# Kernel tuning notes

Hardware: AMD Instinct MI355X
Metric: run time of the kernel (lower is better)

Reference implementation:

```python
import jax, jax.numpy as jnp
import numpy as np

DIM = 128
HEADS = DIM // 8      # mala uses dim//8 heads
HEAD_DIM = 8
HID = int(DIM * 2.66) # 340
B, H, W = 8, 128, 128


def _ln(x, w, b):
    # WithBias LayerNorm over channel dim of NCHW (per-pixel)
    mu = jnp.mean(x, axis=1, keepdims=True)
    var = jnp.mean((x - mu) ** 2, axis=1, keepdims=True)
    return (x - mu) / jnp.sqrt(var + 1e-5) * w[None, :, None, None] + b[None, :, None, None]


def _conv1x1(x, w):
    return jnp.einsum('bchw,oc->bohw', x, w)


def _dwconv(x, w, pad):
    return jax.lax.conv_general_dilated(
        x, w, (1, 1), ((pad, pad), (pad, pad)),
        dimension_numbers=('NCHW', 'OIHW', 'NCHW'),
        feature_group_count=x.shape[1])


def _rope(h, w, head_dim, dtype):
    angle = 1.0 / 10000 ** jnp.linspace(0.0, 1.0, head_dim // 4, dtype=dtype)
    angle = jnp.repeat(angle, 2)                                  # [d/2]
    ih = jnp.arange(h, dtype=dtype)[:, None] * angle[None, :]     # [h, d/2]
    iw = jnp.arange(w, dtype=dtype)[:, None] * angle[None, :]     # [w, d/2]
    d2 = head_dim // 2
    sin = jnp.concatenate([jnp.broadcast_to(jnp.sin(ih)[:, None, :], (h, w, d2)),
                           jnp.broadcast_to(jnp.sin(iw)[None, :, :], (h, w, d2))], -1)
    cos = jnp.concatenate([jnp.broadcast_to(jnp.cos(ih)[:, None, :], (h, w, d2)),
                           jnp.broadcast_to(jnp.cos(iw)[None, :, :], (h, w, d2))], -1)
    return sin.reshape(h * w, head_dim), cos.reshape(h * w, head_dim)


def _rot2(x):
    x1 = x[..., 0::2]
    x2 = x[..., 1::2]
    return jnp.stack([-x2, x1], axis=-1).reshape(x.shape)


def _theta_shift(x, sin, cos):
    return x * cos + _rot2(x) * sin


def setup_inputs() -> dict:
    key = jax.random.key(0)
    ks = jax.random.split(key, 8)
    f = jnp.float32
    return {
        'x': jax.random.normal(ks[0], (B, DIM, H, W), f),
        'ln1_w': jnp.ones((DIM,), f), 'ln1_b': jnp.zeros((DIM,), f),
        'qkvo_w': jax.random.normal(ks[1], (4 * DIM, DIM), f) * (DIM ** -0.5),
        'qkvo_b': jnp.zeros((4 * DIM,), f),
        'lepe_w': jax.random.normal(ks[2], (DIM, 1, 5, 5), f) * 0.2,
        'lepe_b': jnp.zeros((DIM,), f),
        'proj_w': jax.random.normal(ks[3], (DIM, DIM), f) * (DIM ** -0.5),
        'proj_b': jnp.zeros((DIM,), f),
        'ln2_w': jnp.ones((DIM,), f), 'ln2_b': jnp.zeros((DIM,), f),
        'ffn_in_w': jax.random.normal(ks[4], (2 * HID, DIM), f) * (DIM ** -0.5),
        'ffn_dw_w': jax.random.normal(ks[5], (2 * HID, 1, 3, 3), f) * (1.0 / 3.0),
        'ffn_out_w': jax.random.normal(ks[6], (DIM, HID), f) * (HID ** -0.5),
    }


def reference(x, ln1_w, ln1_b, qkvo_w, qkvo_b, lepe_w, lepe_b, proj_w, proj_b,
              ln2_w, ln2_b, ffn_in_w, ffn_dw_w, ffn_out_w):
    Bx, C, Hh, Ww = x.shape
    L = Hh * Ww
    n, d = HEADS, HEAD_DIM
    scale = d ** -0.5

    # --- MALA branch ---
    xn = _ln(x, ln1_w, ln1_b)
    sin, cos = _rope(Hh, Ww, d, x.dtype)
    qkvo = _conv1x1(xn, qkvo_w) + qkvo_b[None, :, None, None]       # [B,4C,H,W]
    qkv, o = qkvo[:, :3 * C], qkvo[:, 3 * C:]
    lepe = _dwconv(qkv[:, 2 * C:], lepe_w, 2) + lepe_b[None, :, None, None]
    t = qkv.reshape(Bx, 3, n, d, L).transpose(1, 0, 2, 4, 3)         # [3,B,n,L,d]
    q = jax.nn.elu(t[0]) + 1.0
    k = jax.nn.elu(t[1]) + 1.0
    v = t[2]
    # z = q @ mean_l(k)^T * scale  (pre-RoPE features)
    z = jnp.einsum('bnld,bnd->bnl', q, jnp.mean(k, axis=2))[..., None] * scale  # [B,n,L,1]
    q = _theta_shift(q, sin, cos)
    k = _theta_shift(k, sin, cos)
    kv = jnp.einsum('bnld,bnle->bnde', k, v) * (scale / L)           # [B,n,d,d]
    res = jnp.einsum('bnld,bnde->bnle', q, kv) * (1.0 + 1.0 / (z + 1e-6)) \
          - z * jnp.mean(v, axis=2, keepdims=True)                   # [B,n,L,d]
    res = res.transpose(0, 1, 3, 2).reshape(Bx, C, Hh, Ww) + lepe
    attn = _conv1x1(res * o, proj_w) + proj_b[None, :, None, None]
    x = x + attn

    # --- gated dwconv FFN ---
    xn2 = _ln(x, ln2_w, ln2_b)
    p = _dwconv(_conv1x1(xn2, ffn_in_w), ffn_dw_w, 1)                # [B,2*HID,H,W]
    x1, x2 = p[:, :HID], p[:, HID:]
    x = x + _conv1x1(jax.nn.gelu(x1, approximate=False) * x2, ffn_out_w)
    return x
```

## Files before the change

### kernel.cpp

```cpp
#include <hip/hip_runtime.h>

#define LSP 16384
#define NBATCH 8
#define NPOS (NBATCH*LSP)
#define NHID 340
#define ATT_SCALE 0.35355339059327373f

#define OFF_A        0ULL
#define OFF_B        33554432ULL
#define OFF_GT2      79691776ULL
#define OFF_C        100663296ULL
#define OFF_PART     134217728ULL
#define OFF_STATS    134381568ULL
#define OFF_SIN      134422528ULL
#define OFF_COS      134946816ULL
#define OFF_WQ       135471104ULL
#define OFF_WQO      135602176ULL
#define OFF_QOB      135667712ULL
#define OFF_WP       135668736ULL
#define OFF_WFI      135701504ULL
#define OFF_WFO      135881728ULL
#define WS_NEEDED    135971840ULL

typedef __attribute__((ext_vector_type(8))) short short8;
typedef __attribute__((ext_vector_type(4))) float floatx4;

__device__ __forceinline__ float bf2f(unsigned short u){
  union { unsigned int i; float f; } c; c.i = ((unsigned int)u) << 16; return c.f;
}
__device__ __forceinline__ unsigned short f2bf(float f){
  union { float f; unsigned int i; } c; c.f = f;
  unsigned int r = c.i + 0x7fffu + ((c.i >> 16) & 1u);
  return (unsigned short)(r >> 16);
}

__device__ __forceinline__ void load_row12(const unsigned short* p, float* r){
  const unsigned int* q = (const unsigned int*)p;
  #pragma unroll
  for (int i=0;i<6;i++){
    unsigned int u = q[i];
    r[2*i]   = bf2f((unsigned short)(u & 0xffffu));
    r[2*i+1] = bf2f((unsigned short)(u >> 16));
  }
}

__device__ __forceinline__ void load_row10(const unsigned short* base, float* r){
  short8 B = *(const short8*)(base + 8);
  r[0] = bf2f(base[7]);
  #pragma unroll
  for (int i=0;i<8;i++) r[1+i] = bf2f((unsigned short)B[i]);
  r[9] = bf2f(base[16]);
}

__global__ void rope_kernel(float* __restrict__ sin_t, float* __restrict__ cos_t){
  int l = blockIdx.x*256 + threadIdx.x;
  if (l >= LSP) return;
  int h = l >> 7, w = l & 127;
  float s0 = sinf((float)h),        c0 = cosf((float)h);
  float s1 = sinf((float)h*1e-4f),  c1 = cosf((float)h*1e-4f);
  float s2 = sinf((float)w),        c2 = cosf((float)w);
  float s3 = sinf((float)w*1e-4f),  c3 = cosf((float)w*1e-4f);
  float* sp = sin_t + l*8; float* cp = cos_t + l*8;
  sp[0]=s0; sp[1]=s0; sp[2]=s1; sp[3]=s1; sp[4]=s2; sp[5]=s2; sp[6]=s3; sp[7]=s3;
  cp[0]=c0; cp[1]=c0; cp[2]=c1; cp[3]=c1; cp[4]=c2; cp[5]=c2; cp[6]=c3; cp[7]=c3;
}

__global__ void wconv_kernel(const float* __restrict__ src, unsigned short* __restrict__ dst,
                             int O, int K, int OP, int KP){
  int i = blockIdx.x*256 + threadIdx.x;
  if (i >= OP*KP) return;
  int o = i / KP, k = i - o*KP;
  float v = (o < O && k < K) ? src[o*K + k] : 0.f;
  dst[i] = f2bf(v);
}

__global__ void reorder_qo_kernel(const float* __restrict__ qkvo_w, const float* __restrict__ qkvo_b,
                                  unsigned short* __restrict__ wqo, float* __restrict__ qo_bias){
  int i = blockIdx.x*256 + threadIdx.x;
  if (i < 256){
    qo_bias[i] = qkvo_b[(i < 128) ? i : i + 256];
  }
  if (i >= 256*128) return;
  int o = i >> 7, k = i & 127;
  int srow = (o < 128) ? o : o + 256;
  wqo[i] = f2bf(qkvo_w[srow*128 + k]);
}

__launch_bounds__(256)
__global__ void ln_kernel(const float* __restrict__ x, const float* __restrict__ gam,
                          const float* __restrict__ bet, unsigned short* __restrict__ out_t){
  __shared__ float ps[2][128], pq[2][128];
  __shared__ unsigned short tile[128*132];
  int t = threadIdx.x;
  int pidx = t & 127;
  int half = t >> 7;
  int p0 = blockIdx.x*128;
  int p = p0 + pidx;
  int b = p >> 14, l = p & 16383;
  const float* xb = x + (((size_t)b) << 21) + (((size_t)(half*64)) << 14) + l;
  float vals[64];
  float s = 0.f, sq = 0.f;
  #pragma unroll
  for (int c = 0; c < 64; c++){
    float v = xb[(size_t)c << 14];
    vals[c] = v;
    s += v; sq += v*v;
  }
  ps[half][pidx] = s; pq[half][pidx] = sq;
  __syncthreads();
  float S = ps[0][pidx] + ps[1][pidx];
  float Q = pq[0][pidx] + pq[1][pidx];
  float mu = S * 0.0078125f;
  float var = Q * 0.0078125f - mu*mu;
  float rstd = rsqrtf(var + 1e-5f);
  #pragma unroll
  for (int c0 = 0; c0 < 64; c0 += 8){
    short8 vv;
    #pragma unroll
    for (int i = 0; i < 8; i++){
      int c = c0 + i;
      int cg = half*64 + c;
      vv[i] = (short)f2bf((vals[c] - mu) * rstd * gam[cg] + bet[cg]);
    }
    *(short8*)&tile[pidx*132 + half*64 + c0] = vv;
  }
  __syncthreads();
  unsigned short* og = out_t + ((size_t)p0 << 7);
  #pragma unroll
  for (int it = 0; it < 8; it++){
    int idx = it*256 + t;
    int row = idx >> 4;
    int col = (idx & 15) * 8;
    *(short8*)&og[(row << 7) + col] = *(const short8*)&tile[row*132 + col];
  }
}

template<int OPAD, int KPAD, bool HASBIAS, bool RESID, bool OUTBF16>
__launch_bounds__(256)
__global__ void gemm_kernel(const unsigned short* __restrict__ in_t,
                            const unsigned short* __restrict__ wb,
                            const float* __restrict__ bias,
                            const float* __restrict__ resid,
                            void* __restrict__ outp){
  constexpr int KS = KPAD / 32;
  constexpr int SBYTES = OUTBF16 ? (64*136*2) : (64*132*4);
  __shared__ __align__(16) unsigned char smem[SBYTES];
  const int l0 = blockIdx.x * 128;
  const int b = l0 >> 14;
  const int lloc0 = l0 & 16383;
  const int t = threadIdx.x;
  const int lane = t & 63;
  const int wv = t >> 6;
  const int lane15 = lane & 15;
  const int quad = lane >> 4;
  const int oc = blockIdx.y;

  short8 fb[2][KS];
  {
    const unsigned short* base = in_t + ((size_t)(l0 + wv*32 + lane15)) * KPAD + quad*8;
    #pragma unroll
    for (int nt = 0; nt < 2; nt++){
      #pragma unroll
      for (int ks = 0; ks < KS; ks++)
        fb[nt][ks] = *(const short8*)(base + (size_t)nt*16*KPAD + ks*32);
    }
  }
  floatx4 acc[4][2];
  #pragma unroll
  for (int mt=0; mt<4; mt++)
    #pragma unroll
    for (int nt=0; nt<2; nt++)
      acc[mt][nt] = (floatx4){0.f,0.f,0.f,0.f};
  #pragma unroll
  for (int ks = 0; ks < KS; ks++){
    short8 fa[4];
    const unsigned short* wrow = wb + ((size_t)(oc*64 + lane15)) * KPAD + ks*32 + quad*8;
    #pragma unroll
    for (int mt=0; mt<4; mt++)
      fa[mt] = *(const short8*)(wrow + (size_t)mt*16*KPAD);
    #pragma unroll
    for (int mt=0; mt<4; mt++)
      #pragma unroll
      for (int nt=0; nt<2; nt++)
        acc[mt][nt] = __builtin_amdgcn_mfma_f32_16x16x32_bf16(fa[mt], fb[nt][ks], acc[mt][nt], 0, 0, 0);
  }

  if (OUTBF16){
    unsigned short* cs = (unsigned short*)smem;
    #pragma unroll
    for (int mt=0; mt<4; mt++)
      #pragma unroll
      for (int nt=0; nt<2; nt++)
        #pragma unroll
        for (int r=0; r<4; r++){
          const int o = mt*16 + quad*4 + r;
          float v = acc[mt][nt][r];
          if (HASBIAS) v += bias[oc*64 + o];
          cs[o*136 + wv*32 + nt*16 + lane15] = f2bf(v);
        }
    __syncthreads();
    unsigned short* og = (unsigned short*)outp;
    #pragma unroll
    for (int j=0; j<4; j++){
      int idx = j*256 + t;
      int row = idx >> 4;
      int col = (idx & 15) * 8;
      short8 v = *(const short8*)&cs[row*136 + col];
      *(short8*)&og[(((size_t)(b*OPAD + oc*64 + row)) << 14) + lloc0 + col] = v;
    }
  } else {
    float* cf = (float*)smem;
    #pragma unroll
    for (int mt=0; mt<4; mt++)
      #pragma unroll
      for (int nt=0; nt<2; nt++)
        #pragma unroll
        for (int r=0; r<4; r++){
          const int o = mt*16 + quad*4 + r;
          float v = acc[mt][nt][r];
          if (HASBIAS) v += bias[oc*64 + o];
          cf[o*132 + wv*32 + nt*16 + lane15] = v;
        }
    __syncthreads();
    float* og = (float*)outp;
    #pragma unroll
    for (int j=0; j<8; j++){
      int idx = j*256 + t;
      int row = idx >> 5;
      int col = (idx & 31) * 4;
      floatx4 v = *(const floatx4*)&cf[row*132 + col];
      if (RESID){
        floatx4 rv = *(const floatx4*)(resid + (((size_t)(b*128 + oc*64 + row)) << 14) + lloc0 + col);
        v += rv;
      }
      *(floatx4*)&og[(((size_t)(b*OPAD + oc*64 + row)) << 14) + lloc0 + col] = v;
    }
  }
}

__launch_bounds__(256)
__global__ void lepe_kernel(const unsigned short* __restrict__ kv,
                            const float* __restrict__ lw, const float* __restrict__ lb,
                            unsigned short* __restrict__ lepe){
  __shared__ unsigned short lds[132*136];
  int bc = blockIdx.x;
  int b = bc >> 7, c = bc & 127;
  int t = threadIdx.x;
  #pragma unroll
  for (int i = t; i < 132*136/8; i += 256)
    *(short8*)(lds + i*8) = (short8){0,0,0,0,0,0,0,0};
  __syncthreads();
  int band = t >> 4, wi = t & 15, w0 = wi*8;
  const unsigned short* vp = kv + (((size_t)(b*256 + 128 + c)) << 14);
  {
    #pragma unroll
    for (int it = 0; it < 8; it++){
      int hh = band + it*16;
      short8 v = *(const short8*)(vp + (hh<<7) + w0);
      unsigned int* dst = (unsigned int*)&lds[(hh+2)*136 + w0 + 2];
      union { short8 s; unsigned int u[4]; } cv; cv.s = v;
      #pragma unroll
      for (int q=0;q<4;q++) dst[q] = cv.u[q];
    }
  }
  float wt[25];
  #pragma unroll
  for (int i=0;i<25;i++) wt[i] = lw[c*25 + i];
  float bias = lb[c];
  __syncthreads();
  int h0 = band*8;
  float win[5][12];
  #pragma unroll
  for (int m=0;m<4;m++) load_row12(&lds[(h0+m)*136 + w0], win[m]);
  unsigned short* outp = lepe + ((size_t)bc << 14);
  #pragma unroll
  for (int s=0;s<8;s++){
    load_row12(&lds[(h0+4+s)*136 + w0], win[(4+s)%5]);
    short8 ov;
    #pragma unroll
    for (int j=0;j<8;j++){
      float acc = bias;
      #pragma unroll
      for (int dy=0;dy<5;dy++){
        const float* r = win[(s+dy)%5];
        #pragma unroll
        for (int dx=0;dx<5;dx++) acc += wt[dy*5+dx]*r[j+dx];
      }
      ov[j] = (short)f2bf(acc);
    }
    *(short8*)(outp + (h0+s)*128 + w0) = ov;
  }
}

__launch_bounds__(256)
__global__ void attn_partial(const unsigned short* __restrict__ kv,
                             const float* __restrict__ sin_t, const float* __restrict__ cos_t,
                             float* __restrict__ partials){
  int pair = blockIdx.x >> 2;
  int chunk = blockIdx.x & 3;
  int b = pair >> 4, hd = pair & 15;
  const unsigned short* kb = kv + (((size_t)(b*256 + hd*8)) << 14);
  const unsigned short* vb = kb + ((size_t)128 << 14);
  float red[80];
  #pragma unroll
  for (int i=0;i<80;i++) red[i]=0.f;
  int l0 = chunk*4096;
  for (int li=0; li<16; li++){
    int l = l0 + li*256 + threadIdx.x;
    float k[8], v[8], ks[8];
    #pragma unroll
    for (int e=0;e<8;e++){
      float t = bf2f(kb[((size_t)e<<14)+l]);
      k[e] = t>0.f ? t+1.f : __expf(t);
      v[e] = bf2f(vb[((size_t)e<<14)+l]);
      red[e]   += k[e];
      red[8+e] += v[e];
    }
    const float* sp = sin_t + l*8;
    const float* cp = cos_t + l*8;
    #pragma unroll
    for (int j=0;j<4;j++){
      float x1=k[2*j], x2=k[2*j+1];
      ks[2*j]   = x1*cp[2*j]   - x2*sp[2*j];
      ks[2*j+1] = x2*cp[2*j+1] + x1*sp[2*j+1];
    }
    #pragma unroll
    for (int d=0; d<8; d++)
      #pragma unroll
      for (int e=0;e<8;e++)
        red[16 + d*8 + e] += ks[d]*v[e];
  }
  #pragma unroll
  for (int off=32; off>0; off>>=1){
    #pragma unroll
    for (int i=0;i<80;i++)
      red[i] += __shfl_down(red[i], off);
  }
  __shared__ float lds[4][80];
  int lane = threadIdx.x & 63, wv = threadIdx.x >> 6;
  if (lane==0){
    #pragma unroll
    for (int i=0;i<80;i++) lds[wv][i] = red[i];
  }
  __syncthreads();
  if (threadIdx.x < 80){
    float s = lds[0][threadIdx.x]+lds[1][threadIdx.x]+lds[2][threadIdx.x]+lds[3][threadIdx.x];
    partials[(size_t)blockIdx.x*80 + threadIdx.x] = s;
  }
}

__global__ void attn_combine(const float* __restrict__ partials, float* __restrict__ stats){
  int i = blockIdx.x*256 + threadIdx.x;
  if (i >= 128*80) return;
  int pair = i / 80, idx = i - pair*80;
  float s = partials[(size_t)(pair*4+0)*80+idx] + partials[(size_t)(pair*4+1)*80+idx]
          + partials[(size_t)(pair*4+2)*80+idx] + partials[(size_t)(pair*4+3)*80+idx];
  s *= (idx < 16) ? (1.f/LSP) : (ATT_SCALE/LSP);
  stats[i] = s;
}

__launch_bounds__(256)
__global__ void attn_apply_kernel(const unsigned short* __restrict__ qo,
                                  const unsigned short* __restrict__ lepe,
                                  const float* __restrict__ stats,
                                  const float* __restrict__ sin_t,
                                  const float* __restrict__ cos_t,
                                  unsigned short* __restrict__ resg_t){
  __shared__ float st[16*80];
  __shared__ unsigned short tile[256*132];
  int p0 = blockIdx.x * 256;
  int b = p0 >> 14;
  for (int i = threadIdx.x; i < 16*80; i += 256) st[i] = stats[b*16*80 + i];
  __syncthreads();
  int t = threadIdx.x;
  int p = p0 + t;
  int l = p & 16383;
  float sv[8], cv[8];
  {
    const float* sp = sin_t + l*8;
    const float* cp = cos_t + l*8;
    #pragma unroll
    for (int i=0;i<8;i++){ sv[i]=sp[i]; cv[i]=cp[i]; }
  }
  #pragma unroll 1
  for (int hd=0; hd<16; hd++){
    const float* S = st + hd*80;
    const unsigned short* qb = qo + (((size_t)(b*256 + hd*8)) << 14) + l;
    const unsigned short* ob = qb + ((size_t)128 << 14);
    const unsigned short* lb = lepe + (((size_t)(b*128 + hd*8)) << 14) + l;
    float q[8];
    #pragma unroll
    for (int e=0;e<8;e++){
      float tq = bf2f(qb[(size_t)e<<14]);
      q[e] = tq > 0.f ? tq + 1.f : __expf(tq);
    }
    float z = 0.f;
    #pragma unroll
    for (int e=0;e<8;e++) z += q[e]*S[e];
    z *= ATT_SCALE;
    float qs[8];
    #pragma unroll
    for (int jj=0;jj<4;jj++){
      float x1=q[2*jj], x2=q[2*jj+1];
      qs[2*jj]   = x1*cv[2*jj]   - x2*sv[2*jj];
      qs[2*jj+1] = x2*cv[2*jj+1] + x1*sv[2*jj+1];
    }
    float fac = 1.f + 1.f/(z + 1e-6f);
    short8 vv;
    #pragma unroll
    for (int e=0;e<8;e++){
      float r = 0.f;
      #pragma unroll
      for (int d=0; d<8; d++) r += qs[d]*S[16 + d*8 + e];
      r = r*fac - z*S[8+e];
      float val = (r + bf2f(lb[(size_t)e<<14])) * bf2f(ob[(size_t)e<<14]);
      vv[e] = (short)f2bf(val);
    }
    *(short8*)&tile[t*132 + hd*8] = vv;
  }
  __syncthreads();
  unsigned short* og = resg_t + ((size_t)p0 << 7);
  #pragma unroll
  for (int it = 0; it < 16; it++){
    int idx = it*256 + t;
    int row = idx >> 4;
    int col = (idx & 15) * 8;
    *(short8*)&og[(row << 7) + col] = *(const short8*)&tile[row*132 + col];
  }
}

#define FPL (66*144)
__launch_bounds__(256)
__global__ void ffn_dwg_kernel(const unsigned short* __restrict__ p,
                               const float* __restrict__ dw,
                               unsigned short* __restrict__ g){
  __shared__ unsigned short lds[2*FPL];
  int bid = blockIdx.x;
  int jc = bid % NHID;
  int rest = bid / NHID;
  int bb = rest & 1;
  int half = rest >> 1;
  int t = threadIdx.x;
  #pragma unroll
  for (int i = t; i < 2*FPL/8; i += 256)
    *(short8*)(lds + i*8) = (short8){0,0,0,0,0,0,0,0};
  __syncthreads();
  int band = t >> 4, wi = t & 15, w0 = wi*8;
  #pragma unroll
  for (int pl=0; pl<2; pl++){
    const unsigned short* src = p + (((size_t)(bb*704 + jc + pl*NHID)) << 14);
    #pragma unroll
    for (int it=0; it<5; it++){
      int r_idx = it*16 + band;
      if (r_idx < 66){
        int h = half*64 - 1 + r_idx;
        if ((unsigned)h < 128u){
          short8 v = *(const short8*)(src + (h<<7) + w0);
          *(short8*)(&lds[pl*FPL + r_idx*144 + w0 + 8]) = v;
        }
      }
    }
  }
  float w1[9], w2[9];
  #pragma unroll
  for (int i=0;i<9;i++){ w1[i] = dw[jc*9 + i]; w2[i] = dw[(jc+NHID)*9 + i]; }
  __syncthreads();
  int rb = band*4;
  float r1[3][10], r2[3][10];
  #pragma unroll
  for (int m=0;m<2;m++){
    load_row10(&lds[(rb+m)*144 + w0], r1[m]);
    load_row10(&lds[FPL + (rb+m)*144 + w0], r2[m]);
  }
  unsigned short* outp = g + (((size_t)(bb*NHID + jc)) << 14);
  #pragma unroll
  for (int s=0;s<4;s++){
    load_row10(&lds[(rb+2+s)*144 + w0], r1[(2+s)%3]);
    load_row10(&lds[FPL + (rb+2+s)*144 + w0], r2[(2+s)%3]);
    int h = half*64 + rb + s;
    short8 ov;
    #pragma unroll
    for (int j=0;j<8;j++){
      float c1 = 0.f, c2 = 0.f;
      #pragma unroll
      for (int dy=0;dy<3;dy++){
        const float* a = r1[(s+dy)%3];
        const float* bpt = r2[(s+dy)%3];
        #pragma unroll
        for (int dx=0;dx<3;dx++){
          c1 += w1[dy*3+dx]*a[j+dx];
          c2 += w2[dy*3+dx]*bpt[j+dx];
        }
      }
      float ge = 0.5f*c1*(1.f + erff(c1*0.70710678118654752f));
      ov[j] = (short)f2bf(ge*c2);
    }
    *(short8*)(outp + h*128 + w0) = ov;
  }
}

__global__ void transpose_g_kernel(const unsigned short* __restrict__ g,
                                   unsigned short* __restrict__ g_t){
  __shared__ unsigned short tile[64][68];
  int bid = blockIdx.x;
  int jt = bid % 6;
  int lt = (bid / 6) & 255;
  int b  = bid / (6*256);
  int j0 = jt*64, l0 = lt*64;
  int t = threadIdx.x;
  {
    int jj = t >> 3;
    int lo = (t & 7) * 8;
    #pragma unroll
    for (int rr=0; rr<2; rr++){
      int j = j0 + jj + rr*32;
      unsigned short vals[8];
      if (j < NHID){
        const unsigned short* src = g + (((size_t)(b*NHID + j)) << 14) + l0 + lo;
        short8 vv = *(const short8*)src;
        #pragma unroll
        for (int i=0;i<8;i++) vals[i] = (unsigned short)vv[i];
      } else {
        #pragma unroll
        for (int i=0;i<8;i++) vals[i] = 0;
      }
      #pragma unroll
      for (int i=0;i<8;i++) tile[lo + i][jj + rr*32] = vals[i];
    }
  }
  __syncthreads();
  {
    int r = t >> 2;
    int c0 = (t & 3)*16;
    int jg = j0 + c0;
    if (jg < 352){
      unsigned short* dst = g_t + ((size_t)(b*LSP + l0 + r))*352 + jg;
      short8 v0, v1;
      #pragma unroll
      for (int i=0;i<8;i++){ v0[i] = (short)tile[r][c0 + i]; v1[i] = (short)tile[r][c0 + 8 + i]; }
      *(short8*)dst = v0;
      *(short8*)(dst+8) = v1;
    }
  }
}

extern "C" void kernel_launch(void* const* d_in, const int* in_sizes, int n_in,
                              void* d_out, int out_size, void* d_ws, size_t ws_size,
                              hipStream_t stream){
  (void)in_sizes; (void)n_in; (void)out_size;
  if (ws_size < WS_NEEDED) return;
  const float* x        = (const float*)d_in[0];
  const float* ln1_w    = (const float*)d_in[1];
  const float* ln1_b    = (const float*)d_in[2];
  const float* qkvo_w   = (const float*)d_in[3];
  const float* qkvo_b   = (const float*)d_in[4];
  const float* lepe_w   = (const float*)d_in[5];
  const float* lepe_b   = (const float*)d_in[6];
  const float* proj_w   = (const float*)d_in[7];
  const float* proj_b   = (const float*)d_in[8];
  const float* ln2_w    = (const float*)d_in[9];
  const float* ln2_b    = (const float*)d_in[10];
  const float* ffn_in_w = (const float*)d_in[11];
  const float* ffn_dw_w = (const float*)d_in[12];
  const float* ffn_out_w= (const float*)d_in[13];

  char* ws = (char*)d_ws;
  unsigned short* bufA   = (unsigned short*)(ws + OFF_A);
  unsigned short* bufB   = (unsigned short*)(ws + OFF_B);
  unsigned short* g_t2   = (unsigned short*)(ws + OFF_GT2);
  unsigned short* lepe   = (unsigned short*)(ws + OFF_C);
  unsigned short* gbuf   = (unsigned short*)(ws + OFF_C);
  float* partials        = (float*)(ws + OFF_PART);
  float* stats           = (float*)(ws + OFF_STATS);
  float* sin_t           = (float*)(ws + OFF_SIN);
  float* cos_t           = (float*)(ws + OFF_COS);
  unsigned short* wq     = (unsigned short*)(ws + OFF_WQ);
  unsigned short* wqo    = (unsigned short*)(ws + OFF_WQO);
  float* qo_bias         = (float*)(ws + OFF_QOB);
  unsigned short* wp     = (unsigned short*)(ws + OFF_WP);
  unsigned short* wfi    = (unsigned short*)(ws + OFF_WFI);
  unsigned short* wfo    = (unsigned short*)(ws + OFF_WFO);
  const unsigned short* wkv = wq + 128*128;

  float* out_f = (float*)d_out;
  dim3 blk(256);
  hipLaunchKernelGGL(rope_kernel, dim3(64), blk, 0, stream, sin_t, cos_t);
  hipLaunchKernelGGL(wconv_kernel, dim3((512*128)/256), blk, 0, stream, qkvo_w, wq, 512,128,512,128);
  hipLaunchKernelGGL(reorder_qo_kernel, dim3((256*128)/256), blk, 0, stream, qkvo_w, qkvo_b, wqo, qo_bias);
  hipLaunchKernelGGL(wconv_kernel, dim3((128*128)/256), blk, 0, stream, proj_w, wp, 128,128,128,128);
  hipLaunchKernelGGL(wconv_kernel, dim3((704*128)/256), blk, 0, stream, ffn_in_w, wfi, 680,128,704,128);
  hipLaunchKernelGGL(wconv_kernel, dim3((128*352)/256), blk, 0, stream, ffn_out_w, wfo, 128,340,128,352);

  hipLaunchKernelGGL(ln_kernel, dim3(1024), blk, 0, stream, x, ln1_w, ln1_b, bufA);
  hipLaunchKernelGGL((gemm_kernel<256,128,true,false,true>), dim3(1024,4), blk, 0, stream,
                     bufA, wkv, qkvo_b + 128, (const float*)nullptr, (void*)bufB);
  hipLaunchKernelGGL(lepe_kernel, dim3(1024), blk, 0, stream, bufB, lepe_w, lepe_b, lepe);
  hipLaunchKernelGGL(attn_partial, dim3(512), blk, 0, stream, bufB, sin_t, cos_t, partials);
  hipLaunchKernelGGL(attn_combine, dim3(40), blk, 0, stream, partials, stats);
  hipLaunchKernelGGL((gemm_kernel<256,128,true,false,true>), dim3(1024,4), blk, 0, stream,
                     bufA, wqo, qo_bias, (const float*)nullptr, (void*)bufB);
  hipLaunchKernelGGL(attn_apply_kernel, dim3(512), blk, 0, stream, bufB, lepe, stats, sin_t, cos_t, bufA);
  hipLaunchKernelGGL((gemm_kernel<128,128,true,true,false>), dim3(1024,2), blk, 0, stream,
                     bufA, wp, proj_b, x, (void*)out_f);

  hipLaunchKernelGGL(ln_kernel, dim3(1024), blk, 0, stream, out_f, ln2_w, ln2_b, bufA);
  for (int bp = 0; bp < 4; bp++){
    const unsigned short* xin = bufA + (size_t)bp*32768*128;
    float* outp = out_f + (size_t)bp*2*128*16384;
    hipLaunchKernelGGL((gemm_kernel<704,128,false,false,true>), dim3(256,11), blk, 0, stream,
                       xin, wfi, (const float*)nullptr, (const float*)nullptr, (void*)bufB);
    hipLaunchKernelGGL(ffn_dwg_kernel, dim3(1360), blk, 0, stream, bufB, ffn_dw_w, gbuf);
    hipLaunchKernelGGL(transpose_g_kernel, dim3(3072), blk, 0, stream, gbuf, g_t2);
    hipLaunchKernelGGL((gemm_kernel<128,352,false,true,false>), dim3(256,2), blk, 0, stream,
                       g_t2, wfo, (const float*)nullptr, outp, (void*)outp);
  }
}
```

Measured before the change: 728.6 us.

## Fuse FFN gate transpose into output GEMM and split attention kernels wider

```diff
diff --git a/kernel.cpp b/kernel.cpp
--- a/kernel.cpp
+++ b/kernel.cpp
@@ -239,6 +239,91 @@
 }
 
 __launch_bounds__(256)
+__global__ void ffn_out_gemm(const unsigned short* __restrict__ g,
+                             const unsigned short* __restrict__ wb,
+                             float* __restrict__ outp){
+  __shared__ __align__(16) unsigned char smem[64*132*4];
+  const int t = threadIdx.x;
+  const int l0 = blockIdx.x * 128;
+  const int b = l0 >> 14;
+  const int lloc0 = l0 & 16383;
+  const int lane = t & 63;
+  const int wv = t >> 6;
+  const int lane15 = lane & 15;
+  const int quad = lane >> 4;
+  const int oc = blockIdx.y;
+  const int jj = t >> 3;
+  const int c8 = t & 7;
+
+  auto stage = [&](int s, int bufi){
+    unsigned short* buf = (unsigned short*)(smem + bufi*10240);
+    int j = s*32 + jj;
+    const unsigned short* src = g + (((size_t)(b*NHID + j)) << 14) + lloc0;
+    #pragma unroll
+    for (int cc=0; cc<2; cc++){
+      int c = c8 + cc*8;
+      short8 v = (short8){0,0,0,0,0,0,0,0};
+      if (j < NHID) v = *(const short8*)(src + c*8);
+      #pragma unroll
+      for (int e=0; e<8; e++)
+        buf[(c*8+e)*40 + jj] = (unsigned short)v[e];
+    }
+  };
+
+  floatx4 acc[4][2];
+  #pragma unroll
+  for (int mt=0; mt<4; mt++)
+    #pragma unroll
+    for (int nt=0; nt<2; nt++)
+      acc[mt][nt] = (floatx4){0.f,0.f,0.f,0.f};
+
+  stage(0, 0);
+  #pragma unroll 1
+  for (int s=0; s<11; s++){
+    __syncthreads();
+    if (s < 10) stage(s+1, (s+1)&1);
+    const unsigned short* cur = (const unsigned short*)(smem + (s&1)*10240);
+    short8 fbv[2];
+    #pragma unroll
+    for (int nt=0; nt<2; nt++)
+      fbv[nt] = *(const short8*)&cur[(wv*32 + nt*16 + lane15)*40 + quad*8];
+    const unsigned short* wrow = wb + ((size_t)(oc*64 + lane15))*352 + s*32 + quad*8;
+    short8 fa[4];
+    #pragma unroll
+    for (int mt=0; mt<4; mt++)
+      fa[mt] = *(const short8*)(wrow + (size_t)mt*16*352);
+    #pragma unroll
+    for (int mt=0; mt<4; mt++)
+      #pragma unroll
+      for (int nt=0; nt<2; nt++)
+        acc[mt][nt] = __builtin_amdgcn_mfma_f32_16x16x32_bf16(fa[mt], fbv[nt], acc[mt][nt], 0, 0, 0);
+  }
+  __syncthreads();
+  float* cf = (float*)smem;
+  #pragma unroll
+  for (int mt=0; mt<4; mt++)
+    #pragma unroll
+    for (int nt=0; nt<2; nt++)
+      #pragma unroll
+      for (int r=0; r<4; r++){
+        const int o = mt*16 + quad*4 + r;
+        cf[o*132 + wv*32 + nt*16 + lane15] = acc[mt][nt][r];
+      }
+  __syncthreads();
+  #pragma unroll
+  for (int j=0; j<8; j++){
+    int idx = j*256 + t;
+    int row = idx >> 5;
+    int col = (idx & 31) * 4;
+    floatx4 v = *(const floatx4*)&cf[row*132 + col];
+    size_t oi = (((size_t)(b*128 + oc*64 + row)) << 14) + lloc0 + col;
+    floatx4 rv = *(const floatx4*)&outp[oi];
+    v += rv;
+    *(floatx4*)&outp[oi] = v;
+  }
+}
+
+__launch_bounds__(256)
 __global__ void lepe_kernel(const unsigned short* __restrict__ kv,
                             const float* __restrict__ lw, const float* __restrict__ lb,
                             unsigned short* __restrict__ lepe){
@@ -296,16 +381,16 @@
 __global__ void attn_partial(const unsigned short* __restrict__ kv,
                              const float* __restrict__ sin_t, const float* __restrict__ cos_t,
                              float* __restrict__ partials){
-  int pair = blockIdx.x >> 2;
-  int chunk = blockIdx.x & 3;
+  int pair = blockIdx.x >> 3;
+  int chunk = blockIdx.x & 7;
   int b = pair >> 4, hd = pair & 15;
   const unsigned short* kb = kv + (((size_t)(b*256 + hd*8)) << 14);
   const unsigned short* vb = kb + ((size_t)128 << 14);
   float red[80];
   #pragma unroll
   for (int i=0;i<80;i++) red[i]=0.f;
-  int l0 = chunk*4096;
-  for (int li=0; li<16; li++){
+  int l0 = chunk*2048;
+  for (int li=0; li<8; li++){
     int l = l0 + li*256 + threadIdx.x;
     float k[8], v[8], ks[8];
     #pragma unroll
@@ -353,8 +438,10 @@
   int i = blockIdx.x*256 + threadIdx.x;
   if (i >= 128*80) return;
   int pair = i / 80, idx = i - pair*80;
-  float s = partials[(size_t)(pair*4+0)*80+idx] + partials[(size_t)(pair*4+1)*80+idx]
-          + partials[(size_t)(pair*4+2)*80+idx] + partials[(size_t)(pair*4+3)*80+idx];
+  float s = 0.f;
+  #pragma unroll
+  for (int cc=0; cc<8; cc++)
+    s += partials[(size_t)(pair*8+cc)*80+idx];
   s *= (idx < 16) ? (1.f/LSP) : (ATT_SCALE/LSP);
   stats[i] = s;
 }
@@ -366,11 +453,12 @@
                                   const float* __restrict__ sin_t,
                                   const float* __restrict__ cos_t,
                                   unsigned short* __restrict__ resg_t){
-  __shared__ float st[16*80];
-  __shared__ unsigned short tile[256*132];
+  __shared__ float st[8*80];
+  __shared__ unsigned short tile[256*66];
   int p0 = blockIdx.x * 256;
   int b = p0 >> 14;
-  for (int i = threadIdx.x; i < 16*80; i += 256) st[i] = stats[b*16*80 + i];
+  int hg = blockIdx.y;
+  for (int i = threadIdx.x; i < 8*80; i += 256) st[i] = stats[b*16*80 + hg*8*80 + i];
   __syncthreads();
   int t = threadIdx.x;
   int p = p0 + t;
@@ -383,8 +471,9 @@
     for (int i=0;i<8;i++){ sv[i]=sp[i]; cv[i]=cp[i]; }
   }
   #pragma unroll 1
-  for (int hd=0; hd<16; hd++){
-    const float* S = st + hd*80;
+  for (int hd8=0; hd8<8; hd8++){
+    int hd = hg*8 + hd8;
+    const float* S = st + hd8*80;
     const unsigned short* qb = qo + (((size_t)(b*256 + hd*8)) << 14) + l;
     const unsigned short* ob = qb + ((size_t)128 << 14);
     const unsigned short* lb = lepe + (((size_t)(b*128 + hd*8)) << 14) + l;
@@ -416,16 +505,16 @@
       float val = (r + bf2f(lb[(size_t)e<<14])) * bf2f(ob[(size_t)e<<14]);
       vv[e] = (short)f2bf(val);
     }
-    *(short8*)&tile[t*132 + hd*8] = vv;
-  }
-  __syncthreads();
-  unsigned short* og = resg_t + ((size_t)p0 << 7);
-  #pragma unroll
-  for (int it = 0; it < 16; it++){
+    *(short8*)&tile[t*66 + hd8*8] = vv;
+  }
+  __syncthreads();
+  unsigned short* og = resg_t + ((size_t)p0 << 7) + hg*64;
+  #pragma unroll
+  for (int it = 0; it < 8; it++){
     int idx = it*256 + t;
-    int row = idx >> 4;
-    int col = (idx & 15) * 8;
-    *(short8*)&og[(row << 7) + col] = *(const short8*)&tile[row*132 + col];
+    int row = idx >> 3;
+    int col = (idx & 7) * 8;
+    *(short8*)&og[(row << 7) + col] = *(const short8*)&tile[row*66 + col];
   }
 }
 
@@ -496,51 +585,6 @@
       ov[j] = (short)f2bf(ge*c2);
     }
     *(short8*)(outp + h*128 + w0) = ov;
-  }
-}
-
-__global__ void transpose_g_kernel(const unsigned short* __restrict__ g,
-                                   unsigned short* __restrict__ g_t){
-  __shared__ unsigned short tile[64][68];
-  int bid = blockIdx.x;
-  int jt = bid % 6;
-  int lt = (bid / 6) & 255;
-  int b  = bid / (6*256);
-  int j0 = jt*64, l0 = lt*64;
-  int t = threadIdx.x;
-  {
-    int jj = t >> 3;
-    int lo = (t & 7) * 8;
-    #pragma unroll
-    for (int rr=0; rr<2; rr++){
-      int j = j0 + jj + rr*32;
-      unsigned short vals[8];
-      if (j < NHID){
-        const unsigned short* src = g + (((size_t)(b*NHID + j)) << 14) + l0 + lo;
-        short8 vv = *(const short8*)src;
-        #pragma unroll
-        for (int i=0;i<8;i++) vals[i] = (unsigned short)vv[i];
-      } else {
-        #pragma unroll
-        for (int i=0;i<8;i++) vals[i] = 0;
-      }
-      #pragma unroll
-      for (int i=0;i<8;i++) tile[lo + i][jj + rr*32] = vals[i];
-    }
-  }
-  __syncthreads();
-  {
-    int r = t >> 2;
-    int c0 = (t & 3)*16;
-    int jg = j0 + c0;
-    if (jg < 352){
-      unsigned short* dst = g_t + ((size_t)(b*LSP + l0 + r))*352 + jg;
-      short8 v0, v1;
-      #pragma unroll
-      for (int i=0;i<8;i++){ v0[i] = (short)tile[r][c0 + i]; v1[i] = (short)tile[r][c0 + 8 + i]; }
-      *(short8*)dst = v0;
-      *(short8*)(dst+8) = v1;
-    }
   }
 }
 
@@ -567,10 +611,9 @@
   char* ws = (char*)d_ws;
   unsigned short* bufA   = (unsigned short*)(ws + OFF_A);
   unsigned short* bufB   = (unsigned short*)(ws + OFF_B);
-  unsigned short* g_t2   = (unsigned short*)(ws + OFF_GT2);
   unsigned short* lepe   = (unsigned short*)(ws + OFF_C);
   unsigned short* gbuf   = (unsigned short*)(ws + OFF_C);
-  float* partials        = (float*)(ws + OFF_PART);
+  float* partials        = (float*)(ws + OFF_GT2);
   float* stats           = (float*)(ws + OFF_STATS);
   float* sin_t           = (float*)(ws + OFF_SIN);
   float* cos_t           = (float*)(ws + OFF_COS);
@@ -595,11 +638,11 @@
   hipLaunchKernelGGL((gemm_kernel<256,128,true,false,true>), dim3(1024,4), blk, 0, stream,
                      bufA, wkv, qkvo_b + 128, (const float*)nullptr, (void*)bufB);
   hipLaunchKernelGGL(lepe_kernel, dim3(1024), blk, 0, stream, bufB, lepe_w, lepe_b, lepe);
-  hipLaunchKernelGGL(attn_partial, dim3(512), blk, 0, stream, bufB, sin_t, cos_t, partials);
+  hipLaunchKernelGGL(attn_partial, dim3(1024), blk, 0, stream, bufB, sin_t, cos_t, partials);
   hipLaunchKernelGGL(attn_combine, dim3(40), blk, 0, stream, partials, stats);
   hipLaunchKernelGGL((gemm_kernel<256,128,true,false,true>), dim3(1024,4), blk, 0, stream,
                      bufA, wqo, qo_bias, (const float*)nullptr, (void*)bufB);
-  hipLaunchKernelGGL(attn_apply_kernel, dim3(512), blk, 0, stream, bufB, lepe, stats, sin_t, cos_t, bufA);
+  hipLaunchKernelGGL(attn_apply_kernel, dim3(512,2), blk, 0, stream, bufB, lepe, stats, sin_t, cos_t, bufA);
   hipLaunchKernelGGL((gemm_kernel<128,128,true,true,false>), dim3(1024,2), blk, 0, stream,
                      bufA, wp, proj_b, x, (void*)out_f);
 
@@ -610,8 +653,6 @@
     hipLaunchKernelGGL((gemm_kernel<704,128,false,false,true>), dim3(256,11), blk, 0, stream,
                        xin, wfi, (const float*)nullptr, (const float*)nullptr, (void*)bufB);
     hipLaunchKernelGGL(ffn_dwg_kernel, dim3(1360), blk, 0, stream, bufB, ffn_dw_w, gbuf);
-    hipLaunchKernelGGL(transpose_g_kernel, dim3(3072), blk, 0, stream, gbuf, g_t2);
-    hipLaunchKernelGGL((gemm_kernel<128,352,false,true,false>), dim3(256,2), blk, 0, stream,
-                       g_t2, wfo, (const float*)nullptr, outp, (void*)outp);
-  }
-}
+    hipLaunchKernelGGL(ffn_out_gemm, dim3(256,2), blk, 0, stream, gbuf, wfo, outp);
+  }
+}
```

Result: no change. 725.6 us (-0.4%).
